# Kernel tuning notes

Measured on AMD Instinct MI355X. Metric: run time of the kernel, lower is better.

Reference implementation:

```python
import jax, jax.numpy as jnp
import numpy as np

N_QUBITS = 20
EVO_SUPPORT = (2, 5)
CHAIN_QUBIT = 0


def _apply_operator(state, op, support):
    """Apply batched operator op (2^k, 2^k, B) to state (2,)*n + (B,) on `support` qubits.

    Faithful to pyqtorch's apply_operator: reshape op to (2,)*2k + (B,) and contract
    the support axes, keeping the batch axis aligned.
    """
    n = state.ndim - 1
    k = len(support)
    B = state.shape[-1]
    op = op.reshape((2,) * (2 * k) + (B,))
    letters = 'abcdefghijklmnopqrstuvwxyz'
    s_l = list(letters[:n])          # state qubit axes
    b = letters[n]                   # batch axis
    out_l = list(letters[n + 1:n + 1 + k])
    in_l = [s_l[q] for q in support]
    op_str = ''.join(out_l) + ''.join(in_l) + b
    st_str = ''.join(s_l) + b
    res = list(s_l)
    for q, o in zip(support, out_l):
        res[q] = o
    return jnp.einsum(f"{op_str},{st_str}->{''.join(res) + b}", op, state)


def setup_inputs() -> dict:
    key = jax.random.key(0)
    ks = jax.random.split(key, 6)
    B = 16
    dim = 2 ** N_QUBITS
    return {
        'state_re': jax.random.normal(ks[0], (dim, B), jnp.float32),
        'state_im': jax.random.normal(ks[1], (dim, B), jnp.float32),
        'hmat_re': jax.random.normal(ks[2], (4, 4, B), jnp.float32),
        'hmat_im': jax.random.normal(ks[3], (4, 4, B), jnp.float32),
        'theta': jax.random.uniform(ks[4], (8, B), jnp.float32),
        'tvals': jax.random.uniform(ks[5], (B,), jnp.float32),
    }


def reference(state_re, state_im, hmat_re, hmat_im, theta, tvals):
    n = N_QUBITS
    B = state_re.shape[-1]
    state = (state_re + 1j * state_im).astype(jnp.complex64).reshape((2,) * n + (B,))

    # --- PyQComposedBlock: chain of single-qubit RX gates composed via reduce(bmm, reversed) ---
    half = 0.5 * theta                      # (N_ops, B)
    c = jnp.cos(half).astype(jnp.complex64)
    s = jnp.sin(half).astype(jnp.complex64)
    # U_k: [[c, -i s], [-i s, c]] per op, batch-first layout (N_ops, B, 2, 2)
    U = jnp.stack([jnp.stack([c, -1j * s], axis=-1),
                   jnp.stack([-1j * s, c], axis=-1)], axis=-2)
    acc = U[-1]
    for i in range(U.shape[0] - 2, -1, -1):  # reduce(bmm, reversed(ops)): U_{N-1} @ ... @ U_0
        acc = acc @ U[i]
    state = _apply_operator(state, jnp.moveaxis(acc, 0, -1), (CHAIN_QUBIT,))

    # --- PyQHamiltonianEvolution: U = exp(-i t H) on a 2-qubit support ---
    A = (hmat_re + 1j * hmat_im).astype(jnp.complex64)       # (4, 4, B)
    H = 0.5 * (A + jnp.conj(jnp.swapaxes(A, 0, 1)))          # Hermitian generator
    Hb = jnp.moveaxis(H, -1, 0)                              # (B, 4, 4)
    evals, V = jnp.linalg.eigh(Hb)                           # H Hermitian -> exact matrix exp
    phase = jnp.exp(-1j * tvals[:, None] * evals)            # (B, 4)
    Ue = jnp.einsum('bij,bj,bkj->bik', V, phase.astype(jnp.complex64), jnp.conj(V))
    state = _apply_operator(state, jnp.moveaxis(Ue, 0, -1), EVO_SUPPORT)

    # --- Observable: total magnetization sum_q Z_q (AddPyQOperation of diagonal Z ops) ---
    w = jnp.zeros((2,) * n, jnp.float32)
    z = jnp.array([1.0, -1.0], jnp.float32)
    for q in range(n):
        w = w + z.reshape((1,) * q + (2,) + (1,) * (n - 1 - q))
    opsi = state * w[..., None]
    # expectation Re<psi|O|psi> per batch element
    return jnp.real(jnp.sum(jnp.conj(state) * opsi, axis=tuple(range(n))))
```

## Files before the change

kernel.cpp:

```cpp
#include <hip/hip_runtime.h>
#include <math.h>

constexpr int NQ     = 20;
constexpr int DIM    = 1 << NQ;
constexpr int B      = 16;
constexpr int GROUPS = 1 << 17;
constexpr int NBLK   = 2048;
constexpr int NTHR   = 256;


__global__ __launch_bounds__(256) void prep_kernel(
    const float* __restrict__ hre, const float* __restrict__ him,
    const float* __restrict__ theta, const float* __restrict__ tv,
    float* __restrict__ ws, float* __restrict__ out) {
  __shared__ double Mre[16][16], Mim[16][16];
  __shared__ double Are[16][16], Aim[16][16];
  __shared__ double Bre[16][16], Bim[16][16];
  __shared__ double nrm[16][4];
  __shared__ int    scl[16];
  __shared__ int    scmax_s;

  int t = threadIdx.x;
  int b = t >> 4, e = t & 15, i = e >> 2, j = e & 3;

  if (t < 16) out[t] = 0.f;
  if (t == 0) scmax_s = 0;

  if (e == 0) {
    double th = 0.0;
    for (int k = 0; k < 8; k++) th += (double)theta[k * B + b];
    th *= 0.5;
    ws[b]     = (float)cos(th);
    ws[B + b] = (float)sin(th);
  }

  {
    double tt  = (double)tv[b];
    double are = hre[(i*4+j)*B + b], aim = him[(i*4+j)*B + b];
    double cre = hre[(j*4+i)*B + b], cim = him[(j*4+i)*B + b];
    double Hre = 0.5*(are + cre), Him = 0.5*(aim - cim);
    Mre[b][e] = tt * Him;
    Mim[b][e] = -tt * Hre;
  }
  __syncthreads();

  if (j == 0) {
    double r = 0.0;
    for (int m = 0; m < 4; m++) r += fabs(Mre[b][i*4+m]) + fabs(Mim[b][i*4+m]);
    nrm[b][i] = r;
  }
  __syncthreads();
  if (e == 0) {
    double ninf = fmax(fmax(nrm[b][0], nrm[b][1]), fmax(nrm[b][2], nrm[b][3]));
    int sc = 0;
    while (ninf > 0.25 && sc < 40) { ninf *= 0.5; sc++; }
    scl[b] = sc;
    atomicMax(&scmax_s, sc);
  }
  __syncthreads();
  int sc = scl[b];
  int scmax = scmax_s;
  {
    double scale = ldexp(1.0, -sc);
    Mre[b][e] *= scale; Mim[b][e] *= scale;
  }
  Are[b][e] = (i == j) ? 1.0 : 0.0;
  Aim[b][e] = 0.0;
  __syncthreads();

  double (*Tr)[16] = Are; double (*Ti)[16] = Aim;
  double (*Pr)[16] = Bre; double (*Pi)[16] = Bim;

  for (int k = 13; k >= 1; k--) {
    double rr = 0.0, ii = 0.0;
    for (int m = 0; m < 4; m++) {
      double mr = Mre[b][i*4+m], mi = Mim[b][i*4+m];
      double xr = Tr[b][m*4+j],  xi = Ti[b][m*4+j];
      rr += mr*xr - mi*xi;
      ii += mr*xi + mi*xr;
    }
    double inv = 1.0 / (double)k;
    Pr[b][e] = rr*inv + ((i == j) ? 1.0 : 0.0);
    Pi[b][e] = ii*inv;
    { double (*s)[16] = Tr; Tr = Pr; Pr = s; s = Ti; Ti = Pi; Pi = s; }
    __syncthreads();
  }
  for (int q = 0; q < scmax; q++) {
    double rr, ii;
    if (q < sc) {
      rr = 0.0; ii = 0.0;
      for (int m = 0; m < 4; m++) {
        double xr = Tr[b][i*4+m], xi = Ti[b][i*4+m];
        double yr = Tr[b][m*4+j], yi = Ti[b][m*4+j];
        rr += xr*yr - xi*yi;
        ii += xr*yi + xi*yr;
      }
    } else { rr = Tr[b][e]; ii = Ti[b][e]; }
    Pr[b][e] = rr; Pi[b][e] = ii;
    { double (*s)[16] = Tr; Tr = Pr; Pr = s; s = Ti; Ti = Pi; Pi = s; }
    __syncthreads();
  }

  float* ue = ws + 2*B + b*32;
  ue[e*2]     = (float)Tr[b][e];
  ue[e*2 + 1] = (float)Ti[b][e];
}

#define RXPAIR(j, f) { \
  float xr = R[j].f, xi = I[j].f, yr = R[(j)+4].f, yi = I[(j)+4].f; \
  R[j].f     = fmaf(c4.f, xr,  s4.f * yi); \
  I[j].f     = fmaf(c4.f, xi, -s4.f * yr); \
  R[(j)+4].f = fmaf(s4.f, xi,  c4.f * yr); \
  I[(j)+4].f = fmaf(c4.f, yi, -s4.f * xr); \
}

#define UE_BI(f, bi, accv) \
  float accv = 0.f; \
  { \
    const float* ub = &u_lds[(b0 + (bi)) * 36]; \
    _Pragma("unroll") \
    for (int k = 0; k < 4; k++) { \
      float4 u0 = *(const float4*)(ub + 8*k);        \
      float4 u1 = *(const float4*)(ub + 8*k + 4);    \
      float rr0 = fmaf(u0.x, R[0].f, -u0.y * I[0].f); \
      rr0 = fmaf(u0.z, R[1].f, rr0); rr0 = fmaf(-u0.w, I[1].f, rr0); \
      rr0 = fmaf(u1.x, R[2].f, rr0); rr0 = fmaf(-u1.y, I[2].f, rr0); \
      rr0 = fmaf(u1.z, R[3].f, rr0); rr0 = fmaf(-u1.w, I[3].f, rr0); \
      float ii0 = fmaf(u0.x, I[0].f, u0.y * R[0].f); \
      ii0 = fmaf(u0.z, I[1].f, ii0); ii0 = fmaf(u0.w, R[1].f, ii0); \
      ii0 = fmaf(u1.x, I[2].f, ii0); ii0 = fmaf(u1.y, R[2].f, ii0); \
      ii0 = fmaf(u1.z, I[3].f, ii0); ii0 = fmaf(u1.w, R[3].f, ii0); \
      float rr1 = fmaf(u0.x, R[4].f, -u0.y * I[4].f); \
      rr1 = fmaf(u0.z, R[5].f, rr1); rr1 = fmaf(-u0.w, I[5].f, rr1); \
      rr1 = fmaf(u1.x, R[6].f, rr1); rr1 = fmaf(-u1.y, I[6].f, rr1); \
      rr1 = fmaf(u1.z, R[7].f, rr1); rr1 = fmaf(-u1.w, I[7].f, rr1); \
      float ii1 = fmaf(u0.x, I[4].f, u0.y * R[4].f); \
      ii1 = fmaf(u0.z, I[5].f, ii1); ii1 = fmaf(u0.w, R[5].f, ii1); \
      ii1 = fmaf(u1.x, I[6].f, ii1); ii1 = fmaf(u1.y, R[6].f, ii1); \
      ii1 = fmaf(u1.z, I[7].f, ii1); ii1 = fmaf(u1.w, R[7].f, ii1); \
      int sb = (k & 1) + (k >> 1); \
      float w0 = wb + (float)(3 - 2*sb);             \
      accv = fmaf(fmaf(rr0, rr0, ii0*ii0), w0,       accv); \
      accv = fmaf(fmaf(rr1, rr1, ii1*ii1), w0 - 2.f, accv); \
    } \
  }

__global__ __launch_bounds__(NTHR, 3) void fused_kernel(
    const float* __restrict__ sre, const float* __restrict__ sim,
    const float* __restrict__ ws, float* __restrict__ out) {
  __shared__ float u_lds[16 * 36];
  __shared__ float cs_lds[32];
  __shared__ float red[16];

  int t = threadIdx.x;
  {
    int bq = t & 15, e2 = t >> 4;
    u_lds[bq * 36 + e2 * 2]     = ws[2 * B + bq * 32 + e2 * 2];
    u_lds[bq * 36 + e2 * 2 + 1] = ws[2 * B + bq * 32 + e2 * 2 + 1];
  }
  if (t < 32) cs_lds[t] = ws[t];
  if (t < 16) red[t] = 0.f;
  __syncthreads();

  int tid = blockIdx.x * NTHR + t;
  int g   = tid >> 2;
  int b0  = (tid & 3) << 2;
  int base = (g & 0x3FFF) | ((g & 0xC000) << 1) | ((g & 0x10000) << 2);
  const float* pr = sre + base * B + b0;
  const float* pi = sim + base * B + b0;

  float4 R[8], I[8];
  #pragma unroll
  for (int j = 0; j < 8; j++) {
    int off = (((((j >> 2) & 1) << 19) | (((j >> 1) & 1) << 17) | ((j & 1) << 14))) * B;
    R[j] = *(const float4*)(pr + off);
    I[j] = *(const float4*)(pi + off);
  }

  float4 c4 = *(const float4*)&cs_lds[b0];
  float4 s4 = *(const float4*)&cs_lds[16 + b0];

  #pragma unroll
  for (int j = 0; j < 4; j++) {
    RXPAIR(j, x) RXPAIR(j, y) RXPAIR(j, z) RXPAIR(j, w)
  }

  int pc = __popc(base);
  float wb = (float)(17 - 2 * pc);

  UE_BI(x, 0, acc0)
  UE_BI(y, 1, acc1)
  UE_BI(z, 2, acc2)
  UE_BI(w, 3, acc3)

  #pragma unroll
  for (int m = 4; m <= 32; m <<= 1) {
    acc0 += __shfl_xor(acc0, m, 64);
    acc1 += __shfl_xor(acc1, m, 64);
    acc2 += __shfl_xor(acc2, m, 64);
    acc3 += __shfl_xor(acc3, m, 64);
  }

  if ((t & 63) < 4) {
    int bb = (t & 3) << 2;
    atomicAdd(&red[bb + 0], acc0);
    atomicAdd(&red[bb + 1], acc1);
    atomicAdd(&red[bb + 2], acc2);
    atomicAdd(&red[bb + 3], acc3);
  }
  __syncthreads();
  if (t < 16) atomicAdd(&out[t], red[t]);
}

extern "C" void kernel_launch(void* const* d_in, const int* in_sizes, int n_in,
                              void* d_out, int out_size, void* d_ws, size_t ws_size,
                              hipStream_t stream) {
  const float* sre = (const float*)d_in[0];
  const float* sim = (const float*)d_in[1];
  const float* hre = (const float*)d_in[2];
  const float* him = (const float*)d_in[3];
  const float* th  = (const float*)d_in[4];
  const float* tv  = (const float*)d_in[5];

  float* ws = (float*)d_ws;
  float* out = (float*)d_out;

  prep_kernel<<<1, 256, 0, stream>>>(hre, him, th, tv, ws, out);
  fused_kernel<<<NBLK, NTHR, 0, stream>>>(sre, sim, ws, out);
}
```

Baseline: 159.2 us.

## Stage state panels through LDS and map one batch element per thread

The fused kernel now loads 32 groups per block cooperatively into shared memory with fully contiguous float4 loads, then each thread takes one (group, batch) pair instead of four batch lanes per thread. The per-batch Ue matrix is kept in registers rather than read from LDS. The goal is to get coalesced global reads and less per-thread register pressure. In exchange it adds a 32KB LDS staging step, a block barrier, and blocks of 512 threads.

```diff
diff --git a/kernel.cpp b/kernel.cpp
--- a/kernel.cpp
+++ b/kernel.cpp
@@ -5,8 +5,9 @@
 constexpr int DIM    = 1 << NQ;
 constexpr int B      = 16;
 constexpr int GROUPS = 1 << 17;
-constexpr int NBLK   = 2048;
-constexpr int NTHR   = 256;
+constexpr int GPB    = 32;
+constexpr int NBLK   = GROUPS / GPB;
+constexpr int NTHR   = 512;
 
 
 __global__ __launch_bounds__(256) void prep_kernel(
@@ -106,108 +107,85 @@
   ue[e*2 + 1] = (float)Ti[b][e];
 }
 
-#define RXPAIR(j, f) { \
-  float xr = R[j].f, xi = I[j].f, yr = R[(j)+4].f, yi = I[(j)+4].f; \
-  R[j].f     = fmaf(c4.f, xr,  s4.f * yi); \
-  I[j].f     = fmaf(c4.f, xi, -s4.f * yr); \
-  R[(j)+4].f = fmaf(s4.f, xi,  c4.f * yr); \
-  I[(j)+4].f = fmaf(c4.f, yi, -s4.f * xr); \
-}
-
-#define UE_BI(f, bi, accv) \
-  float accv = 0.f; \
-  { \
-    const float* ub = &u_lds[(b0 + (bi)) * 36]; \
-    _Pragma("unroll") \
-    for (int k = 0; k < 4; k++) { \
-      float4 u0 = *(const float4*)(ub + 8*k);        \
-      float4 u1 = *(const float4*)(ub + 8*k + 4);    \
-      float rr0 = fmaf(u0.x, R[0].f, -u0.y * I[0].f); \
-      rr0 = fmaf(u0.z, R[1].f, rr0); rr0 = fmaf(-u0.w, I[1].f, rr0); \
-      rr0 = fmaf(u1.x, R[2].f, rr0); rr0 = fmaf(-u1.y, I[2].f, rr0); \
-      rr0 = fmaf(u1.z, R[3].f, rr0); rr0 = fmaf(-u1.w, I[3].f, rr0); \
-      float ii0 = fmaf(u0.x, I[0].f, u0.y * R[0].f); \
-      ii0 = fmaf(u0.z, I[1].f, ii0); ii0 = fmaf(u0.w, R[1].f, ii0); \
-      ii0 = fmaf(u1.x, I[2].f, ii0); ii0 = fmaf(u1.y, R[2].f, ii0); \
-      ii0 = fmaf(u1.z, I[3].f, ii0); ii0 = fmaf(u1.w, R[3].f, ii0); \
-      float rr1 = fmaf(u0.x, R[4].f, -u0.y * I[4].f); \
-      rr1 = fmaf(u0.z, R[5].f, rr1); rr1 = fmaf(-u0.w, I[5].f, rr1); \
-      rr1 = fmaf(u1.x, R[6].f, rr1); rr1 = fmaf(-u1.y, I[6].f, rr1); \
-      rr1 = fmaf(u1.z, R[7].f, rr1); rr1 = fmaf(-u1.w, I[7].f, rr1); \
-      float ii1 = fmaf(u0.x, I[4].f, u0.y * R[4].f); \
-      ii1 = fmaf(u0.z, I[5].f, ii1); ii1 = fmaf(u0.w, R[5].f, ii1); \
-      ii1 = fmaf(u1.x, I[6].f, ii1); ii1 = fmaf(u1.y, R[6].f, ii1); \
-      ii1 = fmaf(u1.z, I[7].f, ii1); ii1 = fmaf(u1.w, R[7].f, ii1); \
-      int sb = (k & 1) + (k >> 1); \
-      float w0 = wb + (float)(3 - 2*sb);             \
-      accv = fmaf(fmaf(rr0, rr0, ii0*ii0), w0,       accv); \
-      accv = fmaf(fmaf(rr1, rr1, ii1*ii1), w0 - 2.f, accv); \
-    } \
-  }
-
-__global__ __launch_bounds__(NTHR, 3) void fused_kernel(
+__global__ __launch_bounds__(NTHR) void fused_kernel(
     const float* __restrict__ sre, const float* __restrict__ sim,
     const float* __restrict__ ws, float* __restrict__ out) {
-  __shared__ float u_lds[16 * 36];
-  __shared__ float cs_lds[32];
+  __shared__ float st[16 * 512];
   __shared__ float red[16];
 
   int t = threadIdx.x;
+  int g0 = blockIdx.x * GPB;
+  int base0 = (g0 & 0x3FFF) | ((g0 & 0xC000) << 1) | ((g0 & 0x10000) << 2);
+
+  #pragma unroll
+  for (int p = 0; p < 4; p++) {
+    int ci    = p * 512 + t;
+    int panel = ci >> 7;
+    int w     = (ci & 127) << 2;
+    int j     = panel >> 1;
+    const float* src = (panel & 1) ? sim : sre;
+    int off = ((((j >> 2) & 1) << 19) | (((j >> 1) & 1) << 17) | ((j & 1) << 14));
+    float4 v = *(const float4*)(src + (base0 + off) * 16 + w);
+    *(float4*)&st[panel * 512 + w] = v;
+  }
+  if (t < 16) red[t] = 0.f;
+
+  int b  = t & 15;
+  int gl = t >> 4;
+  float c = ws[b], s = ws[B + b];
+  float ur[4][4], ui[4][4];
   {
-    int bq = t & 15, e2 = t >> 4;
-    u_lds[bq * 36 + e2 * 2]     = ws[2 * B + bq * 32 + e2 * 2];
-    u_lds[bq * 36 + e2 * 2 + 1] = ws[2 * B + bq * 32 + e2 * 2 + 1];
-  }
-  if (t < 32) cs_lds[t] = ws[t];
-  if (t < 16) red[t] = 0.f;
-  __syncthreads();
-
-  int tid = blockIdx.x * NTHR + t;
-  int g   = tid >> 2;
-  int b0  = (tid & 3) << 2;
-  int base = (g & 0x3FFF) | ((g & 0xC000) << 1) | ((g & 0x10000) << 2);
-  const float* pr = sre + base * B + b0;
-  const float* pi = sim + base * B + b0;
-
-  float4 R[8], I[8];
+    const float* ue = ws + 2 * B + b * 32;
+    #pragma unroll
+    for (int i = 0; i < 4; i++) {
+      float4 p0 = *(const float4*)(ue + i * 8);
+      float4 p1 = *(const float4*)(ue + i * 8 + 4);
+      ur[i][0] = p0.x; ui[i][0] = p0.y; ur[i][1] = p0.z; ui[i][1] = p0.w;
+      ur[i][2] = p1.x; ui[i][2] = p1.y; ur[i][3] = p1.z; ui[i][3] = p1.w;
+    }
+  }
+  __syncthreads();
+
+  float ar[8], ai[8];
   #pragma unroll
   for (int j = 0; j < 8; j++) {
-    int off = (((((j >> 2) & 1) << 19) | (((j >> 1) & 1) << 17) | ((j & 1) << 14))) * B;
-    R[j] = *(const float4*)(pr + off);
-    I[j] = *(const float4*)(pi + off);
-  }
-
-  float4 c4 = *(const float4*)&cs_lds[b0];
-  float4 s4 = *(const float4*)&cs_lds[16 + b0];
+    ar[j] = st[(2 * j) * 512 + t];
+    ai[j] = st[(2 * j + 1) * 512 + t];
+  }
 
   #pragma unroll
   for (int j = 0; j < 4; j++) {
-    RXPAIR(j, x) RXPAIR(j, y) RXPAIR(j, z) RXPAIR(j, w)
-  }
-
+    float xr = ar[j], xi = ai[j], yr = ar[j+4], yi = ai[j+4];
+    ar[j]   = c*xr + s*yi;   ai[j]   = c*xi - s*yr;
+    ar[j+4] = s*xi + c*yr;   ai[j+4] = c*yi - s*xr;
+  }
+
+  int base = base0 + gl;
   int pc = __popc(base);
-  float wb = (float)(17 - 2 * pc);
-
-  UE_BI(x, 0, acc0)
-  UE_BI(y, 1, acc1)
-  UE_BI(z, 2, acc2)
-  UE_BI(w, 3, acc3)
-
-  #pragma unroll
-  for (int m = 4; m <= 32; m <<= 1) {
-    acc0 += __shfl_xor(acc0, m, 64);
-    acc1 += __shfl_xor(acc1, m, 64);
-    acc2 += __shfl_xor(acc2, m, 64);
-    acc3 += __shfl_xor(acc3, m, 64);
-  }
-
-  if ((t & 63) < 4) {
-    int bb = (t & 3) << 2;
-    atomicAdd(&red[bb + 0], acc0);
-    atomicAdd(&red[bb + 1], acc1);
-    atomicAdd(&red[bb + 2], acc2);
-    atomicAdd(&red[bb + 3], acc3);
-  }
+  float wb = (float)(17 - 2*pc);
+  float acc = 0.f;
+  #pragma unroll
+  for (int h = 0; h < 2; h++) {
+    float w0 = wb + (h ? -1.f : 1.f);
+    #pragma unroll
+    for (int k = 0; k < 4; k++) {
+      float rr = 0.f, ii = 0.f;
+      #pragma unroll
+      for (int m = 0; m < 4; m++) {
+        float xr = ar[h*4+m], xi = ai[h*4+m];
+        rr = fmaf(ur[k][m], xr, rr); rr = fmaf(-ui[k][m], xi, rr);
+        ii = fmaf(ur[k][m], xi, ii); ii = fmaf(ui[k][m], xr, ii);
+      }
+      int sb = ((k>>1)&1) + (k&1);
+      float w = w0 + (float)(2 - 2*sb);
+      acc = fmaf(rr*rr + ii*ii, w, acc);
+    }
+  }
+
+  acc += __shfl_xor(acc, 16, 64);
+  acc += __shfl_xor(acc, 32, 64);
+
+  if ((t & 63) < 16) atomicAdd(&red[t & 15], acc);
   __syncthreads();
   if (t < 16) atomicAdd(&out[t], red[t]);
 }
```

Measured after the change: 184.9 us. 1.16x slower.
